# Performance work log

Measured on AMD Instinct MI355X. Metric: run time of the kernel, lower is better.

## Reference

```python
import jax, jax.numpy as jnp
import numpy as np
from jax import lax

N_NODES = 100000
N_EDGES = 1600000
UNITS = 64
DEPTH_EMB = 12
DEPTH_PAR = 5
EPS = 1e-5


def setup_inputs() -> dict:
    key = jax.random.key(0)
    ks = jax.random.split(key, 24)
    x = jax.random.normal(ks[0], (N_NODES, 1), dtype=jnp.float32)
    edge_index = jax.random.randint(ks[1], (2, N_EDGES), 0, N_NODES, dtype=jnp.int32)
    s = 1.0 / np.sqrt(UNITS)
    # GCN conv params: first layer maps feats=1 -> 64, remaining 11 map 64 -> 64
    conv_w0 = jax.random.normal(ks[2], (1, UNITS), dtype=jnp.float32)
    conv_w = jax.random.normal(ks[3], (DEPTH_EMB - 1, UNITS, UNITS), dtype=jnp.float32) * s
    conv_b = jnp.zeros((DEPTH_EMB, UNITS), dtype=jnp.float32)
    # GraphNorm params (applied after every conv except the last)
    gn_gamma = jnp.ones((DEPTH_EMB - 1, UNITS), dtype=jnp.float32)
    gn_beta = jnp.zeros((DEPTH_EMB - 1, UNITS), dtype=jnp.float32)
    gn_alpha = jnp.ones((DEPTH_EMB - 1, UNITS), dtype=jnp.float32)
    # ParNet heads: 4 residual 64->64 linears + final 64->1
    phe_w = jax.random.normal(ks[4], (DEPTH_PAR - 1, UNITS, UNITS), dtype=jnp.float32) * s
    phe_b = jnp.zeros((DEPTH_PAR - 1, UNITS), dtype=jnp.float32)
    phe_wl = jax.random.normal(ks[5], (UNITS, 1), dtype=jnp.float32) * s
    phe_bl = jnp.zeros((1,), dtype=jnp.float32)
    heu_w = jax.random.normal(ks[6], (DEPTH_PAR - 1, UNITS, UNITS), dtype=jnp.float32) * s
    heu_b = jnp.zeros((DEPTH_PAR - 1, UNITS), dtype=jnp.float32)
    heu_wl = jax.random.normal(ks[7], (UNITS, 1), dtype=jnp.float32) * s
    heu_bl = jnp.zeros((1,), dtype=jnp.float32)
    return {"x": x, "edge_index": edge_index,
            "conv_w0": conv_w0, "conv_w": conv_w, "conv_b": conv_b,
            "gn_gamma": gn_gamma, "gn_beta": gn_beta, "gn_alpha": gn_alpha,
            "phe_w": phe_w, "phe_b": phe_b, "phe_wl": phe_wl, "phe_bl": phe_bl,
            "heu_w": heu_w, "heu_b": heu_b, "heu_wl": heu_wl, "heu_bl": heu_bl}


def _graph_norm(h, gamma, beta, alpha):
    # single-graph GraphNorm: per-feature mean over nodes, mean-scale alpha
    mean = jnp.mean(h, axis=0, keepdims=True)            # [1, C]
    hc = h - alpha * mean
    var = jnp.mean(hc * hc, axis=0, keepdims=True)       # [1, C]
    return gamma * hc * lax.rsqrt(var + EPS) + beta


def _parnet(h, ws, bs, wl, bl):
    for i in range(DEPTH_PAR - 1):
        h = jax.nn.relu(h + h @ ws[i] + bs[i])
    return jax.nn.sigmoid(h @ wl + bl)[:, 0]             # [N]


def reference(x, edge_index, conv_w0, conv_w, conv_b, gn_gamma, gn_beta, gn_alpha,
              phe_w, phe_b, phe_wl, phe_bl, heu_w, heu_b, heu_wl, heu_bl):
    n = x.shape[0]
    src, dst = edge_index[0], edge_index[1]
    # GCN symmetric normalization with self-loops
    deg = 1.0 + jax.ops.segment_sum(jnp.ones_like(src, dtype=x.dtype), dst, num_segments=n)
    dinv = lax.rsqrt(deg)                                # [N]
    norm_e = (dinv[src] * dinv[dst])[:, None]            # [E, 1]
    self_norm = (dinv * dinv)[:, None]                   # [N, 1]

    h = x
    for i in range(DEPTH_EMB):
        w = conv_w0 if i == 0 else conv_w[i - 1]
        h = h @ w                                        # [N, 64]
        agg = jax.ops.segment_sum(h[src] * norm_e, dst, num_segments=n)
        h = agg + h * self_norm + conv_b[i]
        if i < DEPTH_EMB - 1:
            h = _graph_norm(h, gn_gamma[i], gn_beta[i], gn_alpha[i])
            h = jax.nn.silu(h)

    phe = _parnet(h, phe_w, phe_b, phe_wl, phe_bl)
    heu = _parnet(h, heu_w, heu_b, heu_wl, heu_bl)
    return (phe, heu)
```

## Files before the change

kernel.cpp:

```cpp
#include <hip/hip_runtime.h>
#include <hip/hip_bf16.h>
#include <hip/hip_fp16.h>
#include <math.h>

#define UNITS 64
#define DEPTH_EMB 12
#define DEPTH_PAR 5
#define GN_EPS 1e-5f
#define NFILLB 256
#define MAXNB 512


__global__ void k_deg(const int* __restrict__ dst, int* __restrict__ cnt, int E) {
    int e = blockIdx.x * blockDim.x + threadIdx.x;
    if (e < E) atomicAdd(&cnt[dst[e]], 1);
}

__global__ void k_dinv(const int* __restrict__ cnt, float* __restrict__ dinv, int n) {
    int i = blockIdx.x * blockDim.x + threadIdx.x;
    if (i < n) dinv[i] = rsqrtf(1.0f + (float)cnt[i]);
}

__global__ void k_chunksum(const int* __restrict__ cnt, int* __restrict__ csum, int n) {
    __shared__ int sd[256];
    int base = blockIdx.x * 1024;
    int s = 0;
    for (int i = threadIdx.x; i < 1024; i += 256) {
        int idx = base + i;
        if (idx < n) s += cnt[idx];
    }
    sd[threadIdx.x] = s;
    __syncthreads();
    for (int off = 128; off > 0; off >>= 1) {
        if (threadIdx.x < off) sd[threadIdx.x] += sd[threadIdx.x + off];
        __syncthreads();
    }
    if (threadIdx.x == 0) csum[blockIdx.x] = sd[0];
}

__global__ void k_scansum(const int* __restrict__ csum, int* __restrict__ coff,
                          int* __restrict__ rowptr, int nchunks) {
    __shared__ int sd[256];
    int tid = threadIdx.x;
    int v = (tid < nchunks) ? csum[tid] : 0;
    sd[tid] = v;
    __syncthreads();
    for (int off = 1; off < 256; off <<= 1) {
        int t = (tid >= off) ? sd[tid - off] : 0;
        __syncthreads();
        sd[tid] += t;
        __syncthreads();
    }
    if (tid < nchunks) coff[tid] = sd[tid] - v;
    if (tid == 0) rowptr[0] = 0;
}

__global__ void k_scanfinal(const int* __restrict__ cnt, const int* __restrict__ coff,
                            int* __restrict__ rowptr, int n) {
    __shared__ int sd[1024];
    int base = blockIdx.x * 1024;
    int tid = threadIdx.x;
    int idx = base + tid;
    int v = (idx < n) ? cnt[idx] : 0;
    sd[tid] = v;
    __syncthreads();
    for (int off = 1; off < 1024; off <<= 1) {
        int t = (tid >= off) ? sd[tid - off] : 0;
        __syncthreads();
        sd[tid] += t;
        __syncthreads();
    }
    if (idx < n) rowptr[idx + 1] = coff[blockIdx.x] + sd[tid];
}


__global__ void k_bcount(const int* __restrict__ dst, int* __restrict__ table,
                         int E, int nb, int epb) {
    __shared__ int hist[MAXNB];
    int tid = threadIdx.x;
    for (int i = tid; i < nb; i += 256) hist[i] = 0;
    __syncthreads();
    int e0 = blockIdx.x * epb;
    int e1 = min(e0 + epb, E);
    for (int e = e0 + tid; e < e1; e += 256) atomicAdd(&hist[dst[e] >> 8], 1);
    __syncthreads();
    for (int i = tid; i < nb; i += 256) table[i * NFILLB + blockIdx.x] = hist[i];
}

__global__ void k_bscan(int* __restrict__ table, int* __restrict__ btot) {
    __shared__ int sd[NFILLB];
    int b = blockIdx.x;
    int tid = threadIdx.x;
    int v = table[b * NFILLB + tid];
    sd[tid] = v;
    __syncthreads();
    for (int off = 1; off < NFILLB; off <<= 1) {
        int t = (tid >= off) ? sd[tid - off] : 0;
        __syncthreads();
        sd[tid] += t;
        __syncthreads();
    }
    table[b * NFILLB + tid] = sd[tid] - v;
    if (tid == NFILLB - 1) btot[b] = sd[NFILLB - 1];
}

__global__ void k_boffscan(const int* __restrict__ btot, int* __restrict__ boff, int nb) {
    __shared__ int sd[MAXNB];
    int tid = threadIdx.x;
    int v = (tid < nb) ? btot[tid] : 0;
    sd[tid] = v;
    __syncthreads();
    for (int off = 1; off < MAXNB; off <<= 1) {
        int t = (tid >= off) ? sd[tid - off] : 0;
        __syncthreads();
        sd[tid] += t;
        __syncthreads();
    }
    if (tid < nb) boff[tid] = sd[tid] - v;
}

__global__ void k_bscatter(const int* __restrict__ src, const int* __restrict__ dst,
                           const int* __restrict__ table, const int* __restrict__ boff,
                           unsigned long long* __restrict__ pairs, int E, int nb, int epb) {
    __shared__ int hist[MAXNB];
    int tid = threadIdx.x;
    for (int i = tid; i < nb; i += 256) hist[i] = 0;
    __syncthreads();
    int e0 = blockIdx.x * epb;
    int e1 = min(e0 + epb, E);
    for (int e = e0 + tid; e < e1; e += 256) {
        int d = dst[e];
        int b = d >> 8;
        int local = atomicAdd(&hist[b], 1);
        int p = boff[b] + table[b * NFILLB + blockIdx.x] + local;
        pairs[p] = ((unsigned long long)(unsigned)d << 32) | (unsigned)src[e];
    }
}

__global__ void k_pfill(const unsigned long long* __restrict__ pairs,
                        const int* __restrict__ rowptr, int* __restrict__ fillc,
                        int* __restrict__ srcs, int E) {
    int stride = gridDim.x * blockDim.x;
    for (int idx = blockIdx.x * blockDim.x + threadIdx.x; idx < E; idx += stride) {
        unsigned long long pr = pairs[idx];
        int s = (int)(pr & 0xffffffffu);
        int d = (int)(pr >> 32);
        int p = rowptr[d] + atomicAdd(&fillc[d], 1);
        srcs[p] = s;
    }
}


__global__ void k_l0(const float* __restrict__ x, const float* __restrict__ w0,
                     const float* __restrict__ dinv, __half* __restrict__ h2, int n) {
    int gid = blockIdx.x * blockDim.x + threadIdx.x;
    if (gid >= n * UNITS) return;
    int node = gid >> 6, c = gid & 63;
    h2[gid] = __float2half(x[node] * w0[c] * dinv[node]);
}


template <int DO_STATS>
__global__ void k_gather(const __half* __restrict__ h2, float* __restrict__ h,
                         const int* __restrict__ rowptr, const int* __restrict__ srcs,
                         const float* __restrict__ dinv, const float* __restrict__ b,
                         float* __restrict__ stats, int n) {
    int lane = threadIdx.x & 63;
    int wib = threadIdx.x >> 6;
    int wpb = blockDim.x >> 6;
    int gwave = blockIdx.x * wpb + wib;
    int nwaves = gridDim.x * wpb;
    float bj = b[lane];
    float s1 = 0.0f, s2 = 0.0f;

    for (int nd = gwave; nd < n; nd += nwaves) {
        int node = __builtin_amdgcn_readfirstlane(nd);
        int beg = rowptr[node], end = rowptr[node + 1];
        float di = dinv[node];
        float acc0 = __half2float(h2[(size_t)node * UNITS + lane]);
        float acc1 = 0.0f, acc2 = 0.0f, acc3 = 0.0f;
        int j = beg;
        for (; j + 8 <= end; j += 8) {
            int i0 = srcs[j + 0], i1 = srcs[j + 1], i2 = srcs[j + 2], i3 = srcs[j + 3];
            int i4 = srcs[j + 4], i5 = srcs[j + 5], i6 = srcs[j + 6], i7 = srcs[j + 7];
            float v0 = __half2float(h2[(size_t)i0 * UNITS + lane]);
            float v1 = __half2float(h2[(size_t)i1 * UNITS + lane]);
            float v2 = __half2float(h2[(size_t)i2 * UNITS + lane]);
            float v3 = __half2float(h2[(size_t)i3 * UNITS + lane]);
            float v4 = __half2float(h2[(size_t)i4 * UNITS + lane]);
            float v5 = __half2float(h2[(size_t)i5 * UNITS + lane]);
            float v6 = __half2float(h2[(size_t)i6 * UNITS + lane]);
            float v7 = __half2float(h2[(size_t)i7 * UNITS + lane]);
            acc0 += v0; acc1 += v1; acc2 += v2; acc3 += v3;
            acc0 += v4; acc1 += v5; acc2 += v6; acc3 += v7;
        }
        for (; j + 4 <= end; j += 4) {
            int i0 = srcs[j + 0], i1 = srcs[j + 1], i2 = srcs[j + 2], i3 = srcs[j + 3];
            float v0 = __half2float(h2[(size_t)i0 * UNITS + lane]);
            float v1 = __half2float(h2[(size_t)i1 * UNITS + lane]);
            float v2 = __half2float(h2[(size_t)i2 * UNITS + lane]);
            float v3 = __half2float(h2[(size_t)i3 * UNITS + lane]);
            acc0 += v0; acc1 += v1; acc2 += v2; acc3 += v3;
        }
        for (; j < end; ++j) acc0 += __half2float(h2[(size_t)srcs[j] * UNITS + lane]);
        float acc = (acc0 + acc1) + (acc2 + acc3);
        float hv = fmaf(acc, di, bj);
        h[(size_t)node * UNITS + lane] = hv;
        if (DO_STATS) {
            s1 += hv;
            s2 = fmaf(hv, hv, s2);
        }
    }

    if (DO_STATS) {
        __shared__ float sd[2][4][UNITS];
        sd[0][wib][lane] = s1;
        sd[1][wib][lane] = s2;
        __syncthreads();
        if (threadIdx.x < UNITS) {
            float a1 = 0.0f, a2 = 0.0f;
            for (int r = 0; r < wpb; ++r) {
                a1 += sd[0][r][lane];
                a2 += sd[1][r][lane];
            }
            atomicAdd(&stats[lane], a1);
            atomicAdd(&stats[UNITS + lane], a2);
        }
    }
}


__global__ void k_nsl(const float* __restrict__ in, __half* __restrict__ out,
                      const float* __restrict__ W, const float* __restrict__ dinv,
                      const float* __restrict__ stats, const float* __restrict__ gamma,
                      const float* __restrict__ beta, const float* __restrict__ alpha,
                      float inv_n, int n) {
    __shared__ float lds[4][UNITS];
    int lane = threadIdx.x & 63;
    int wib = threadIdx.x >> 6;
    int wpb = blockDim.x >> 6;
    int gwave = blockIdx.x * wpb + wib;
    int nwaves = gridDim.x * wpb;

    float w[UNITS];
#pragma unroll
    for (int k = 0; k < UNITS; ++k) w[k] = W[k * UNITS + lane];

    float m = stats[lane] * inv_n;
    float ex2 = stats[UNITS + lane] * inv_n;
    float al = alpha[lane];
    float var = ex2 - m * m * (2.0f * al - al * al);
    float g = gamma[lane] * rsqrtf(var + GN_EPS);
    float A = g;
    float B = beta[lane] - g * al * m;

    for (int nd = gwave; nd < n; nd += nwaves) {
        int node = __builtin_amdgcn_readfirstlane(nd);
        float hv = in[(size_t)node * UNITS + lane];
        float t = fmaf(hv, A, B);
        t = t / (1.0f + __expf(-t));
        lds[wib][lane] = t;
        float di = dinv[node];
        float a0 = 0.0f, a1 = 0.0f, a2 = 0.0f, a3 = 0.0f;
#pragma unroll
        for (int k = 0; k < UNITS; k += 4) {
            float4 tv = *(const float4*)&lds[wib][k];
            a0 = fmaf(tv.x, w[k + 0], a0);
            a1 = fmaf(tv.y, w[k + 1], a1);
            a2 = fmaf(tv.z, w[k + 2], a2);
            a3 = fmaf(tv.w, w[k + 3], a3);
        }
        float acc = (a0 + a1) + (a2 + a3);
        out[(size_t)node * UNITS + lane] = __float2half(acc * di);
    }
}


__global__ void k_linear_par(const float* __restrict__ in, float* __restrict__ out,
                             const float* __restrict__ W, const float* __restrict__ b, int n) {
    int lane = threadIdx.x & 63;
    int wib = threadIdx.x >> 6;
    int wpb = blockDim.x >> 6;
    int gwave = blockIdx.x * wpb + wib;
    int nwaves = gridDim.x * wpb;

    float w[UNITS];
#pragma unroll
    for (int k = 0; k < UNITS; ++k) w[k] = W[k * UNITS + lane];
    float bj = b[lane];

    for (int nd = gwave; nd < n; nd += nwaves) {
        int node = __builtin_amdgcn_readfirstlane(nd);
        const float* __restrict__ row = in + (size_t)node * UNITS;
        float a0 = 0.0f, a1 = 0.0f, a2 = 0.0f, a3 = 0.0f;
#pragma unroll
        for (int k = 0; k < UNITS; k += 4) {
            a0 = fmaf(row[k + 0], w[k + 0], a0);
            a1 = fmaf(row[k + 1], w[k + 1], a1);
            a2 = fmaf(row[k + 2], w[k + 2], a2);
            a3 = fmaf(row[k + 3], w[k + 3], a3);
        }
        float acc = (a0 + a1) + (a2 + a3) + row[lane] + bj;
        acc = fmaxf(acc, 0.0f);
        out[(size_t)node * UNITS + lane] = acc;
    }
}


__global__ void k_linear_head(const float* __restrict__ in, const float* __restrict__ W,
                              const float* __restrict__ b, const float* __restrict__ wl,
                              const float* __restrict__ bl, float* __restrict__ out, int n) {
    int lane = threadIdx.x & 63;
    int wib = threadIdx.x >> 6;
    int wpb = blockDim.x >> 6;
    int gwave = blockIdx.x * wpb + wib;
    int nwaves = gridDim.x * wpb;

    float w[UNITS];
#pragma unroll
    for (int k = 0; k < UNITS; ++k) w[k] = W[k * UNITS + lane];
    float bj = b[lane];
    float wv = wl[lane];
    float blv = bl[0];

    for (int nd = gwave; nd < n; nd += nwaves) {
        int node = __builtin_amdgcn_readfirstlane(nd);
        const float* __restrict__ row = in + (size_t)node * UNITS;
        float a0 = 0.0f, a1 = 0.0f, a2 = 0.0f, a3 = 0.0f;
#pragma unroll
        for (int k = 0; k < UNITS; k += 4) {
            a0 = fmaf(row[k + 0], w[k + 0], a0);
            a1 = fmaf(row[k + 1], w[k + 1], a1);
            a2 = fmaf(row[k + 2], w[k + 2], a2);
            a3 = fmaf(row[k + 3], w[k + 3], a3);
        }
        float acc = (a0 + a1) + (a2 + a3) + row[lane] + bj;
        acc = fmaxf(acc, 0.0f);
        float p = acc * wv;
#pragma unroll
        for (int off = 32; off > 0; off >>= 1) p += __shfl_xor(p, off, 64);
        if (lane == 0) out[node] = 1.0f / (1.0f + __expf(-(p + blv)));
    }
}


extern "C" void kernel_launch(void* const* d_in, const int* in_sizes, int n_in,
                              void* d_out, int out_size, void* d_ws, size_t ws_size,
                              hipStream_t stream) {
    const float* x = (const float*)d_in[0];
    const int* ei = (const int*)d_in[1];
    const float* conv_w0 = (const float*)d_in[2];
    const float* conv_w = (const float*)d_in[3];
    const float* conv_b = (const float*)d_in[4];
    const float* gn_gamma = (const float*)d_in[5];
    const float* gn_beta = (const float*)d_in[6];
    const float* gn_alpha = (const float*)d_in[7];
    const float* phe_w = (const float*)d_in[8];
    const float* phe_b = (const float*)d_in[9];
    const float* phe_wl = (const float*)d_in[10];
    const float* phe_bl = (const float*)d_in[11];
    const float* heu_w = (const float*)d_in[12];
    const float* heu_b = (const float*)d_in[13];
    const float* heu_wl = (const float*)d_in[14];
    const float* heu_bl = (const float*)d_in[15];

    const int N = in_sizes[0];
    const int E = in_sizes[1] / 2;
    const int NC = N * UNITS;
    const int NCHUNK1024 = (N + 1023) / 1024;
    const int NB = (N + 255) / 256;
    const int EPB = (E + NFILLB - 1) / NFILLB;

    const int* src = ei;
    const int* dstp = ei + E;

    char* w = (char*)d_ws;
    float* dinv = (float*)w;  w += (size_t)N * 4;
    float* h = (float*)w;     w += (size_t)NC * 4;
    float* hx = (float*)w;    w += (size_t)NC * 4;
    float* h3 = (float*)w;    w += (size_t)NC * 4;
    float* stats = (float*)w; w += (size_t)DEPTH_EMB * 128 * 4;
    int* cnt = (int*)w;       w += (size_t)N * 4;
    int* rowptr = (int*)w;    w += (size_t)(N + 1) * 4;
    int* fillc = (int*)w;     w += (size_t)N * 4;
    int* srcs = (int*)w;      w += (size_t)(E + 16) * 4;
    int* csum = (int*)w;      w += 256 * 4;
    int* coff = (int*)w;      w += 256 * 4;
    int* table = (int*)w;     w += (size_t)MAXNB * NFILLB * 4;
    int* btot = (int*)w;      w += MAXNB * 4;
    int* boff = (int*)w;      w += MAXNB * 4;

    __half* h2 = (__half*)hx;
    unsigned long long* pairs = (unsigned long long*)h3;
    float* out = (float*)d_out;

    const int B = 256;
    const int gE = (E + B - 1) / B;
    const int gN = (N + B - 1) / B;
    const int gNC = (NC + B - 1) / B;

    hipMemsetAsync(cnt, 0, (size_t)N * 4, stream);
    hipMemsetAsync(fillc, 0, (size_t)N * 4, stream);
    hipMemsetAsync(stats, 0, (size_t)DEPTH_EMB * 128 * 4, stream);
    k_deg<<<gE, B, 0, stream>>>(dstp, cnt, E);
    k_dinv<<<gN, B, 0, stream>>>(cnt, dinv, N);
    k_chunksum<<<NCHUNK1024, 256, 0, stream>>>(cnt, csum, N);
    k_scansum<<<1, 256, 0, stream>>>(csum, coff, rowptr, NCHUNK1024);
    k_scanfinal<<<NCHUNK1024, 1024, 0, stream>>>(cnt, coff, rowptr, N);
    k_bcount<<<NFILLB, 256, 0, stream>>>(dstp, table, E, NB, EPB);
    k_bscan<<<NB, NFILLB, 0, stream>>>(table, btot);
    k_boffscan<<<1, MAXNB, 0, stream>>>(btot, boff, NB);
    k_bscatter<<<NFILLB, 256, 0, stream>>>(src, dstp, table, boff, pairs, E, NB, EPB);
    k_pfill<<<2048, B, 0, stream>>>(pairs, rowptr, fillc, srcs, E);

    k_l0<<<gNC, B, 0, stream>>>(x, conv_w0, dinv, h2, N);
    for (int i = 0; i < DEPTH_EMB; ++i) {
        float* st = stats + (size_t)i * 128;
        if (i < DEPTH_EMB - 1) {
            k_gather<1><<<2048, B, 0, stream>>>(h2, h, rowptr, srcs, dinv,
                                                conv_b + (size_t)i * UNITS, st, N);
            k_nsl<<<2048, B, 0, stream>>>(h, h2, conv_w + (size_t)i * UNITS * UNITS,
                                          dinv, st,
                                          gn_gamma + (size_t)i * UNITS,
                                          gn_beta + (size_t)i * UNITS,
                                          gn_alpha + (size_t)i * UNITS,
                                          1.0f / (float)N, N);
        } else {
            k_gather<0><<<2048, B, 0, stream>>>(h2, h, rowptr, srcs, dinv,
                                                conv_b + (size_t)i * UNITS, st, N);
        }
    }

    for (int head = 0; head < 2; ++head) {
        const float* wsrc = head == 0 ? phe_w : heu_w;
        const float* bsrc = head == 0 ? phe_b : heu_b;
        const float* wl = head == 0 ? phe_wl : heu_wl;
        const float* bl = head == 0 ? phe_bl : heu_bl;
        float* o = out + (size_t)head * N;

        k_linear_par<<<2048, B, 0, stream>>>(h, h3, wsrc, bsrc, N);
        k_linear_par<<<2048, B, 0, stream>>>(h3, hx, wsrc + (size_t)1 * UNITS * UNITS,
                                             bsrc + (size_t)1 * UNITS, N);
        k_linear_par<<<2048, B, 0, stream>>>(hx, h3, wsrc + (size_t)2 * UNITS * UNITS,
                                             bsrc + (size_t)2 * UNITS, N);
        k_linear_head<<<2048, B, 0, stream>>>(h3, wsrc + (size_t)3 * UNITS * UNITS,
                                              bsrc + (size_t)3 * UNITS, wl, bl, o, N);
    }
}
```

Baseline: 1.534 ms.

## Split CSR adjacency into four source-range segments per destination node

Edges are bucketed by (source range, destination) with four source ranges. The CSR build (degree count, scans, bucket scatter, fill) now works over 4N keys, and the gather walks four sub-rows per node. The aim is better cache locality for the gathered source rows by grouping neighbours by source range. The cost is a larger preprocessing pass, four rowptr lookups per node and shorter inner loops that make less use of the 8-way unroll. Because every node still visits all four ranges in the same pass, the locality gain may be small.

```diff
diff --git a/kernel.cpp b/kernel.cpp
--- a/kernel.cpp
+++ b/kernel.cpp
@@ -7,8 +7,9 @@
 #define DEPTH_EMB 12
 #define DEPTH_PAR 5
 #define GN_EPS 1e-5f
+#define NRANGE 4
 #define NFILLB 256
-#define MAXNB 512
+#define MAXB 1600
 
 
 __global__ void k_deg(const int* __restrict__ dst, int* __restrict__ cnt, int E) {
@@ -19,6 +20,14 @@
 __global__ void k_dinv(const int* __restrict__ cnt, float* __restrict__ dinv, int n) {
     int i = blockIdx.x * blockDim.x + threadIdx.x;
     if (i < n) dinv[i] = rsqrtf(1.0f + (float)cnt[i]);
+}
+
+__global__ void k_deg4(const int* __restrict__ src, const int* __restrict__ dst,
+                       int* __restrict__ cnt4, int E, int n, int rdiv) {
+    int e = blockIdx.x * blockDim.x + threadIdx.x;
+    if (e >= E) return;
+    int r = src[e] / rdiv;
+    atomicAdd(&cnt4[r * n + dst[e]], 1);
 }
 
 __global__ void k_chunksum(const int* __restrict__ cnt, int* __restrict__ csum, int n) {
@@ -40,12 +49,12 @@
 
 __global__ void k_scansum(const int* __restrict__ csum, int* __restrict__ coff,
                           int* __restrict__ rowptr, int nchunks) {
-    __shared__ int sd[256];
+    __shared__ int sd[512];
     int tid = threadIdx.x;
     int v = (tid < nchunks) ? csum[tid] : 0;
     sd[tid] = v;
     __syncthreads();
-    for (int off = 1; off < 256; off <<= 1) {
+    for (int off = 1; off < 512; off <<= 1) {
         int t = (tid >= off) ? sd[tid - off] : 0;
         __syncthreads();
         sd[tid] += t;
@@ -74,15 +83,19 @@
 }
 
 
-__global__ void k_bcount(const int* __restrict__ dst, int* __restrict__ table,
-                         int E, int nb, int epb) {
-    __shared__ int hist[MAXNB];
+__global__ void k_bcount(const int* __restrict__ src, const int* __restrict__ dst,
+                         int* __restrict__ table, int E, int nb, int epb,
+                         int n, int rdiv) {
+    __shared__ int hist[MAXB];
     int tid = threadIdx.x;
     for (int i = tid; i < nb; i += 256) hist[i] = 0;
     __syncthreads();
     int e0 = blockIdx.x * epb;
     int e1 = min(e0 + epb, E);
-    for (int e = e0 + tid; e < e1; e += 256) atomicAdd(&hist[dst[e] >> 8], 1);
+    for (int e = e0 + tid; e < e1; e += 256) {
+        int k = (src[e] / rdiv) * n + dst[e];
+        atomicAdd(&hist[k >> 8], 1);
+    }
     __syncthreads();
     for (int i = tid; i < nb; i += 256) table[i * NFILLB + blockIdx.x] = hist[i];
 }
@@ -105,47 +118,62 @@
 }
 
 __global__ void k_boffscan(const int* __restrict__ btot, int* __restrict__ boff, int nb) {
-    __shared__ int sd[MAXNB];
-    int tid = threadIdx.x;
-    int v = (tid < nb) ? btot[tid] : 0;
-    sd[tid] = v;
-    __syncthreads();
-    for (int off = 1; off < MAXNB; off <<= 1) {
+    __shared__ int sd[512];
+    int tid = threadIdx.x;
+    int v[4];
+    int s = 0;
+#pragma unroll
+    for (int q = 0; q < 4; ++q) {
+        int i = tid * 4 + q;
+        v[q] = (i < nb) ? btot[i] : 0;
+        s += v[q];
+    }
+    sd[tid] = s;
+    __syncthreads();
+    for (int off = 1; off < 512; off <<= 1) {
         int t = (tid >= off) ? sd[tid - off] : 0;
         __syncthreads();
         sd[tid] += t;
         __syncthreads();
     }
-    if (tid < nb) boff[tid] = sd[tid] - v;
+    int excl = sd[tid] - s;
+#pragma unroll
+    for (int q = 0; q < 4; ++q) {
+        int i = tid * 4 + q;
+        if (i < nb) boff[i] = excl;
+        excl += v[q];
+    }
 }
 
 __global__ void k_bscatter(const int* __restrict__ src, const int* __restrict__ dst,
                            const int* __restrict__ table, const int* __restrict__ boff,
-                           unsigned long long* __restrict__ pairs, int E, int nb, int epb) {
-    __shared__ int hist[MAXNB];
+                           unsigned long long* __restrict__ pairs, int E, int nb, int epb,
+                           int n, int rdiv) {
+    __shared__ int hist[MAXB];
     int tid = threadIdx.x;
     for (int i = tid; i < nb; i += 256) hist[i] = 0;
     __syncthreads();
     int e0 = blockIdx.x * epb;
     int e1 = min(e0 + epb, E);
     for (int e = e0 + tid; e < e1; e += 256) {
-        int d = dst[e];
-        int b = d >> 8;
+        int s = src[e];
+        int k = (s / rdiv) * n + dst[e];
+        int b = k >> 8;
         int local = atomicAdd(&hist[b], 1);
         int p = boff[b] + table[b * NFILLB + blockIdx.x] + local;
-        pairs[p] = ((unsigned long long)(unsigned)d << 32) | (unsigned)src[e];
+        pairs[p] = ((unsigned long long)(unsigned)k << 32) | (unsigned)s;
     }
 }
 
 __global__ void k_pfill(const unsigned long long* __restrict__ pairs,
-                        const int* __restrict__ rowptr, int* __restrict__ fillc,
+                        const int* __restrict__ rowptr4, int* __restrict__ fill4,
                         int* __restrict__ srcs, int E) {
     int stride = gridDim.x * blockDim.x;
     for (int idx = blockIdx.x * blockDim.x + threadIdx.x; idx < E; idx += stride) {
         unsigned long long pr = pairs[idx];
         int s = (int)(pr & 0xffffffffu);
-        int d = (int)(pr >> 32);
-        int p = rowptr[d] + atomicAdd(&fillc[d], 1);
+        int k = (int)(pr >> 32);
+        int p = rowptr4[k] + atomicAdd(&fill4[k], 1);
         srcs[p] = s;
     }
 }
@@ -162,7 +190,7 @@
 
 template <int DO_STATS>
 __global__ void k_gather(const __half* __restrict__ h2, float* __restrict__ h,
-                         const int* __restrict__ rowptr, const int* __restrict__ srcs,
+                         const int* __restrict__ rowptr4, const int* __restrict__ srcs,
                          const float* __restrict__ dinv, const float* __restrict__ b,
                          float* __restrict__ stats, int n) {
     int lane = threadIdx.x & 63;
@@ -175,34 +203,37 @@
 
     for (int nd = gwave; nd < n; nd += nwaves) {
         int node = __builtin_amdgcn_readfirstlane(nd);
-        int beg = rowptr[node], end = rowptr[node + 1];
         float di = dinv[node];
         float acc0 = __half2float(h2[(size_t)node * UNITS + lane]);
         float acc1 = 0.0f, acc2 = 0.0f, acc3 = 0.0f;
-        int j = beg;
-        for (; j + 8 <= end; j += 8) {
-            int i0 = srcs[j + 0], i1 = srcs[j + 1], i2 = srcs[j + 2], i3 = srcs[j + 3];
-            int i4 = srcs[j + 4], i5 = srcs[j + 5], i6 = srcs[j + 6], i7 = srcs[j + 7];
-            float v0 = __half2float(h2[(size_t)i0 * UNITS + lane]);
-            float v1 = __half2float(h2[(size_t)i1 * UNITS + lane]);
-            float v2 = __half2float(h2[(size_t)i2 * UNITS + lane]);
-            float v3 = __half2float(h2[(size_t)i3 * UNITS + lane]);
-            float v4 = __half2float(h2[(size_t)i4 * UNITS + lane]);
-            float v5 = __half2float(h2[(size_t)i5 * UNITS + lane]);
-            float v6 = __half2float(h2[(size_t)i6 * UNITS + lane]);
-            float v7 = __half2float(h2[(size_t)i7 * UNITS + lane]);
-            acc0 += v0; acc1 += v1; acc2 += v2; acc3 += v3;
-            acc0 += v4; acc1 += v5; acc2 += v6; acc3 += v7;
-        }
-        for (; j + 4 <= end; j += 4) {
-            int i0 = srcs[j + 0], i1 = srcs[j + 1], i2 = srcs[j + 2], i3 = srcs[j + 3];
-            float v0 = __half2float(h2[(size_t)i0 * UNITS + lane]);
-            float v1 = __half2float(h2[(size_t)i1 * UNITS + lane]);
-            float v2 = __half2float(h2[(size_t)i2 * UNITS + lane]);
-            float v3 = __half2float(h2[(size_t)i3 * UNITS + lane]);
-            acc0 += v0; acc1 += v1; acc2 += v2; acc3 += v3;
-        }
-        for (; j < end; ++j) acc0 += __half2float(h2[(size_t)srcs[j] * UNITS + lane]);
+        for (int r = 0; r < NRANGE; ++r) {
+            int base = r * n + node;
+            int beg = rowptr4[base], end = rowptr4[base + 1];
+            int j = beg;
+            for (; j + 8 <= end; j += 8) {
+                int i0 = srcs[j + 0], i1 = srcs[j + 1], i2 = srcs[j + 2], i3 = srcs[j + 3];
+                int i4 = srcs[j + 4], i5 = srcs[j + 5], i6 = srcs[j + 6], i7 = srcs[j + 7];
+                float v0 = __half2float(h2[(size_t)i0 * UNITS + lane]);
+                float v1 = __half2float(h2[(size_t)i1 * UNITS + lane]);
+                float v2 = __half2float(h2[(size_t)i2 * UNITS + lane]);
+                float v3 = __half2float(h2[(size_t)i3 * UNITS + lane]);
+                float v4 = __half2float(h2[(size_t)i4 * UNITS + lane]);
+                float v5 = __half2float(h2[(size_t)i5 * UNITS + lane]);
+                float v6 = __half2float(h2[(size_t)i6 * UNITS + lane]);
+                float v7 = __half2float(h2[(size_t)i7 * UNITS + lane]);
+                acc0 += v0; acc1 += v1; acc2 += v2; acc3 += v3;
+                acc0 += v4; acc1 += v5; acc2 += v6; acc3 += v7;
+            }
+            for (; j + 4 <= end; j += 4) {
+                int i0 = srcs[j + 0], i1 = srcs[j + 1], i2 = srcs[j + 2], i3 = srcs[j + 3];
+                float v0 = __half2float(h2[(size_t)i0 * UNITS + lane]);
+                float v1 = __half2float(h2[(size_t)i1 * UNITS + lane]);
+                float v2 = __half2float(h2[(size_t)i2 * UNITS + lane]);
+                float v3 = __half2float(h2[(size_t)i3 * UNITS + lane]);
+                acc0 += v0; acc1 += v1; acc2 += v2; acc3 += v3;
+            }
+            for (; j < end; ++j) acc0 += __half2float(h2[(size_t)srcs[j] * UNITS + lane]);
+        }
         float acc = (acc0 + acc1) + (acc2 + acc3);
         float hv = fmaf(acc, di, bj);
         h[(size_t)node * UNITS + lane] = hv;
@@ -367,8 +398,10 @@
     const int N = in_sizes[0];
     const int E = in_sizes[1] / 2;
     const int NC = N * UNITS;
-    const int NCHUNK1024 = (N + 1023) / 1024;
-    const int NB = (N + 255) / 256;
+    const int N4 = NRANGE * N;
+    const int RDIV = (N + NRANGE - 1) / NRANGE;
+    const int NCHUNK4 = (N4 + 1023) / 1024;
+    const int NB = (N4 + 255) / 256;
     const int EPB = (E + NFILLB - 1) / NFILLB;
 
     const int* src = ei;
@@ -381,14 +414,15 @@
     float* h3 = (float*)w;    w += (size_t)NC * 4;
     float* stats = (float*)w; w += (size_t)DEPTH_EMB * 128 * 4;
     int* cnt = (int*)w;       w += (size_t)N * 4;
-    int* rowptr = (int*)w;    w += (size_t)(N + 1) * 4;
-    int* fillc = (int*)w;     w += (size_t)N * 4;
+    int* cnt4 = (int*)w;      w += (size_t)N4 * 4;
+    int* rowptr4 = (int*)w;   w += (size_t)(N4 + 1) * 4;
+    int* fill4 = (int*)w;     w += (size_t)N4 * 4;
     int* srcs = (int*)w;      w += (size_t)(E + 16) * 4;
-    int* csum = (int*)w;      w += 256 * 4;
-    int* coff = (int*)w;      w += 256 * 4;
-    int* table = (int*)w;     w += (size_t)MAXNB * NFILLB * 4;
-    int* btot = (int*)w;      w += MAXNB * 4;
-    int* boff = (int*)w;      w += MAXNB * 4;
+    int* csum = (int*)w;      w += 512 * 4;
+    int* coff = (int*)w;      w += 512 * 4;
+    int* table = (int*)w;     w += (size_t)MAXB * NFILLB * 4;
+    int* btot = (int*)w;      w += MAXB * 4;
+    int* boff = (int*)w;      w += MAXB * 4;
 
     __half* h2 = (__half*)hx;
     unsigned long long* pairs = (unsigned long long*)h3;
@@ -400,24 +434,26 @@
     const int gNC = (NC + B - 1) / B;
 
     hipMemsetAsync(cnt, 0, (size_t)N * 4, stream);
-    hipMemsetAsync(fillc, 0, (size_t)N * 4, stream);
+    hipMemsetAsync(cnt4, 0, (size_t)N4 * 4, stream);
+    hipMemsetAsync(fill4, 0, (size_t)N4 * 4, stream);
     hipMemsetAsync(stats, 0, (size_t)DEPTH_EMB * 128 * 4, stream);
     k_deg<<<gE, B, 0, stream>>>(dstp, cnt, E);
     k_dinv<<<gN, B, 0, stream>>>(cnt, dinv, N);
-    k_chunksum<<<NCHUNK1024, 256, 0, stream>>>(cnt, csum, N);
-    k_scansum<<<1, 256, 0, stream>>>(csum, coff, rowptr, NCHUNK1024);
-    k_scanfinal<<<NCHUNK1024, 1024, 0, stream>>>(cnt, coff, rowptr, N);
-    k_bcount<<<NFILLB, 256, 0, stream>>>(dstp, table, E, NB, EPB);
+    k_deg4<<<gE, B, 0, stream>>>(src, dstp, cnt4, E, N, RDIV);
+    k_chunksum<<<NCHUNK4, 256, 0, stream>>>(cnt4, csum, N4);
+    k_scansum<<<1, 512, 0, stream>>>(csum, coff, rowptr4, NCHUNK4);
+    k_scanfinal<<<NCHUNK4, 1024, 0, stream>>>(cnt4, coff, rowptr4, N4);
+    k_bcount<<<NFILLB, 256, 0, stream>>>(src, dstp, table, E, NB, EPB, N, RDIV);
     k_bscan<<<NB, NFILLB, 0, stream>>>(table, btot);
-    k_boffscan<<<1, MAXNB, 0, stream>>>(btot, boff, NB);
-    k_bscatter<<<NFILLB, 256, 0, stream>>>(src, dstp, table, boff, pairs, E, NB, EPB);
-    k_pfill<<<2048, B, 0, stream>>>(pairs, rowptr, fillc, srcs, E);
+    k_boffscan<<<1, 512, 0, stream>>>(btot, boff, NB);
+    k_bscatter<<<NFILLB, 256, 0, stream>>>(src, dstp, table, boff, pairs, E, NB, EPB, N, RDIV);
+    k_pfill<<<2048, B, 0, stream>>>(pairs, rowptr4, fill4, srcs, E);
 
     k_l0<<<gNC, B, 0, stream>>>(x, conv_w0, dinv, h2, N);
     for (int i = 0; i < DEPTH_EMB; ++i) {
         float* st = stats + (size_t)i * 128;
         if (i < DEPTH_EMB - 1) {
-            k_gather<1><<<2048, B, 0, stream>>>(h2, h, rowptr, srcs, dinv,
+            k_gather<1><<<2048, B, 0, stream>>>(h2, h, rowptr4, srcs, dinv,
                                                 conv_b + (size_t)i * UNITS, st, N);
             k_nsl<<<2048, B, 0, stream>>>(h, h2, conv_w + (size_t)i * UNITS * UNITS,
                                           dinv, st,
@@ -426,7 +462,7 @@
                                           gn_alpha + (size_t)i * UNITS,
                                           1.0f / (float)N, N);
         } else {
-            k_gather<0><<<2048, B, 0, stream>>>(h2, h, rowptr, srcs, dinv,
+            k_gather<0><<<2048, B, 0, stream>>>(h2, h, rowptr4, srcs, dinv,
                                                 conv_b + (size_t)i * UNITS, st, N);
         }
     }
```

Result: slower. 1.883 ms (+22.8%).
